# Optimization experiments

Hardware: AMD Instinct MI355X
Metric: run time of the kernel (lower is better)

The kernel has to match this reference:

```python
import jax, jax.numpy as jnp
import numpy as np

N = 50000        # nodes
E = 800000       # edges (before self-loops)
IN_DIM = 128
OUT_DIM = 128
HEADS = 4
HEAD_DIM = OUT_DIM // HEADS
NEG_SLOPE = 0.2  # GATv2Conv default negative_slope
LN_EPS = 1e-5


def setup_inputs() -> dict:
    key = jax.random.key(0)
    ks = jax.random.split(key, 6)
    def glorot(k, shape, fan):
        return jax.random.normal(k, shape, jnp.float32) * (1.0 / np.sqrt(fan))
    x = jax.random.normal(ks[0], (N, IN_DIM), jnp.float32)
    edge_index = jax.random.randint(ks[1], (2, E), 0, N, dtype=jnp.int32)
    W_l = glorot(ks[2], (IN_DIM, OUT_DIM), IN_DIM)   # lin_l (source/message transform)
    W_r = glorot(ks[3], (IN_DIM, OUT_DIM), IN_DIM)   # lin_r (target transform)
    att = glorot(ks[4], (HEADS, HEAD_DIM), HEAD_DIM)  # per-head attention vector a
    bias = jnp.zeros((OUT_DIM,), jnp.float32)
    gamma = jnp.ones((OUT_DIM,), jnp.float32)
    beta = jnp.zeros((OUT_DIM,), jnp.float32)
    return {"x": x, "edge_index": edge_index, "W_l": W_l, "W_r": W_r,
            "att": att, "bias": bias, "gamma": gamma, "beta": beta}


def reference(x, edge_index, W_l, W_r, att, bias, gamma, beta):
    # --- GATv2Conv (PyG defaults: add_self_loops=True, share_weights=False) ---
    loop = jnp.arange(N, dtype=edge_index.dtype)
    src = jnp.concatenate([edge_index[0], loop])  # message sources j
    dst = jnp.concatenate([edge_index[1], loop])  # message targets i

    xl = (x @ W_l).reshape(N, HEADS, HEAD_DIM)  # source-side features
    xr = (x @ W_r).reshape(N, HEADS, HEAD_DIM)  # target-side features

    h = xl[src] + xr[dst]                                  # [E+N, H, D]
    h = jnp.where(h > 0, h, NEG_SLOPE * h)                 # LeakyReLU
    logits = jnp.einsum('ehd,hd->eh', h, att)              # [E+N, H]

    # segment softmax over incoming edges of each target node
    m = jax.ops.segment_max(logits, dst, num_segments=N)   # [N, H]
    p = jnp.exp(logits - m[dst])
    s = jax.ops.segment_sum(p, dst, num_segments=N)        # [N, H]
    alpha = p / s[dst]                                     # [E+N, H]

    out = jax.ops.segment_sum(alpha[:, :, None] * xl[src], dst, num_segments=N)
    out = out.reshape(N, OUT_DIM) + bias                   # concat heads + bias

    # --- ELU + LayerNorm ---
    out = jax.nn.elu(out)
    mu = jnp.mean(out, axis=-1, keepdims=True)
    var = jnp.var(out, axis=-1, keepdims=True)
    out = (out - mu) / jnp.sqrt(var + LN_EPS) * gamma + beta
    return out
```

## Files before the change

### kernel.cpp

```cpp
#include <hip/hip_runtime.h>

#define IN_DIM   128
#define OUT_DIM  128
#define HEADS    4
#define HEAD_DIM 32
#define NEG_SLOPE 0.2f
#define LN_EPS    1e-5f
#define CAP      64
#define CAP_SH   6
#define BIN_EDGES 4096

typedef __bf16 bf16x8 __attribute__((ext_vector_type(8)));
typedef float  f32x4  __attribute__((ext_vector_type(4)));

__device__ __forceinline__ unsigned short f2bf(float f) {
    unsigned u = __float_as_uint(f);
    u += 0x7fffu + ((u >> 16) & 1u);
    return (unsigned short)(u >> 16);
}

__device__ __forceinline__ float2 bf2up(unsigned u) {
    return make_float2(__uint_as_float(u << 16), __uint_as_float(u & 0xffff0000u));
}
__device__ __forceinline__ float2 pk_add(float2 a, float2 b) {
    return make_float2(a.x + b.x, a.y + b.y);
}
__device__ __forceinline__ float2 pk_max(float2 a, float2 b) {
    return make_float2(fmaxf(a.x, b.x), fmaxf(a.y, b.y));
}
__device__ __forceinline__ float2 pk_muls(float2 a, float s) {
    return make_float2(a.x * s, a.y * s);
}
__device__ __forceinline__ float2 pk_fma(float2 a, float2 b, float2 c) {
    return make_float2(fmaf(a.x, b.x, c.x), fmaf(a.y, b.y, c.y));
}
__device__ __forceinline__ float2 pk_fmas(float s, float2 b, float2 c) {
    return make_float2(fmaf(s, b.x, c.x), fmaf(s, b.y, c.y));
}

__global__ void prep0(const float* __restrict__ Wl,
                      const float* __restrict__ Wr,
                      unsigned short* __restrict__ wpack,
                      int* __restrict__ cnt, int N) {
    const int tid = blockIdx.x * 256 + threadIdx.x;
    for (int i = tid; i < N + 8; i += 4096) cnt[i] = 0;

    const int lane = tid & 63;
    const int ks   = (tid >> 6) & 3;
    const int t    = tid >> 8;
    const int nt   = t & 7, half = t >> 3;
    const int n    = nt * 16 + (lane & 15);
    const int k0   = ks * 32 + (lane >> 4) * 8;
    const float* W = half ? Wr : Wl;
    union { unsigned short s[8]; uint4 q; } u;
    #pragma unroll
    for (int j = 0; j < 8; ++j) u.s[j] = f2bf(W[(k0 + j) * OUT_DIM + n]);
    ((uint4*)wpack)[tid] = u.q;
}

__global__ void bin_edges(const int* __restrict__ ei, int E, int N,
                          unsigned* __restrict__ buf, int bufstride,
                          int* __restrict__ pcur) {
    __shared__ int lhist[8], lbase[8];
    if (threadIdx.x < 8) lhist[threadIdx.x] = 0;
    __syncthreads();
    const int ET  = E + N;
    const int seg = blockIdx.x * BIN_EDGES;
    unsigned pr[16], rk[16];
    #pragma unroll
    for (int j = 0; j < 16; ++j) {
        const int e = seg + j * 256 + threadIdx.x;
        rk[j] = 0xffffffffu;
        if (e < ET) {
            int src, dst;
            if (e < E) { dst = ei[E + e]; src = ei[e]; }
            else       { dst = src = e - E; }
            const int p = dst >> 13;
            pr[j] = ((unsigned)dst << 16) | (unsigned)src;
            const int r = atomicAdd(&lhist[p], 1);
            rk[j] = ((unsigned)p << 16) | (unsigned)r;
        }
    }
    __syncthreads();
    if (threadIdx.x < 8)
        lbase[threadIdx.x] = atomicAdd(&pcur[threadIdx.x], lhist[threadIdx.x]);
    __syncthreads();
    #pragma unroll
    for (int j = 0; j < 16; ++j) {
        if (rk[j] != 0xffffffffu) {
            const int p = rk[j] >> 16, r = rk[j] & 0xffffu;
            buf[(size_t)p * bufstride + lbase[p] + r] = pr[j];
        }
    }
}

__global__ void scatter_gemm(const unsigned* __restrict__ buf, int bufstride,
                             const int* __restrict__ pcur,
                             int* __restrict__ cnt,
                             unsigned short* __restrict__ csr16,
                             const float* __restrict__ x,
                             const unsigned short* __restrict__ wpack,
                             unsigned short* __restrict__ xl,
                             unsigned short* __restrict__ xr,
                             int N) {
    if (blockIdx.x < 512) {
        const int p  = blockIdx.x & 7;
        const int bi = blockIdx.x >> 3;
        const int pc = pcur[p];
        const unsigned* b = buf + (size_t)p * bufstride;
        for (int i = bi * 256 + threadIdx.x; i < pc; i += 64 * 256) {
            const unsigned pair = b[i];
            const int dst = (int)(pair >> 16);
            const int src = (int)(pair & 0xffffu);
            const int pos = atomicAdd(&cnt[dst], 1);
            if (pos < CAP) csr16[(dst << CAP_SH) + pos] = (unsigned short)src;
        }
        return;
    }

    const int bid    = blockIdx.x - 512;
    const int wv     = threadIdx.x >> 6;
    const int lane   = threadIdx.x & 63;
    const int rowgrp = wv & 1, half = wv >> 1;
    const int r0     = bid * 32 + rowgrp * 16;
    const int m      = lane & 15, quad = lane >> 4;
    const int r      = r0 + m;
    unsigned short* out = half ? xr : xl;
    const uint4* wp = (const uint4*)wpack;

    f32x4 acc[8];
    #pragma unroll
    for (int nt = 0; nt < 8; ++nt) acc[nt] = (f32x4){0.f, 0.f, 0.f, 0.f};

    #pragma unroll
    for (int ks = 0; ks < 4; ++ks) {
        union { unsigned short s[8]; bf16x8 v; } af;
        if (r < N) {
            const float4* xp = (const float4*)(x + (size_t)r * IN_DIM + ks * 32 + quad * 8);
            float4 f0 = xp[0];
            float4 f1 = xp[1];
            af.s[0] = f2bf(f0.x); af.s[1] = f2bf(f0.y);
            af.s[2] = f2bf(f0.z); af.s[3] = f2bf(f0.w);
            af.s[4] = f2bf(f1.x); af.s[5] = f2bf(f1.y);
            af.s[6] = f2bf(f1.z); af.s[7] = f2bf(f1.w);
        } else {
            #pragma unroll
            for (int j = 0; j < 8; ++j) af.s[j] = 0;
        }
        #pragma unroll
        for (int nt = 0; nt < 8; ++nt) {
            union { uint4 q; bf16x8 v; } bf_;
            bf_.q = wp[((half * 8 + nt) * 4 + ks) * 64 + lane];
            acc[nt] = __builtin_amdgcn_mfma_f32_16x16x32_bf16(af.v, bf_.v, acc[nt], 0, 0, 0);
        }
    }

    #pragma unroll
    for (int nt = 0; nt < 8; ++nt) {
        #pragma unroll
        for (int i = 0; i < 4; ++i) {
            int gr = r0 + quad * 4 + i;
            if (gr < N) out[(size_t)gr * OUT_DIM + nt * 16 + m] = f2bf(acc[nt][i]);
        }
    }
}

__global__ void aggregate(const int* __restrict__ cnt,
                          const unsigned short* __restrict__ csr16,
                          const uint4* __restrict__ xlq,
                          const uint4* __restrict__ xrq,
                          const float* __restrict__ att,
                          const float* __restrict__ bias,
                          const float* __restrict__ gamma,
                          const float* __restrict__ beta,
                          float* __restrict__ out, int N) {
    const int node = (int)((blockIdx.x * (size_t)blockDim.x + threadIdx.x) >> 6);
    const int lane = threadIdx.x & 63;
    if (node >= N) return;
    const int slot = lane >> 4;
    const int sl   = lane & 15;

    int deg = cnt[node];
    deg = (deg > CAP) ? CAP : deg;
    const int beg = node << CAP_SH;

    const uint4 urq = xrq[(size_t)node * 16 + sl];
    float2 r2[4] = { bf2up(urq.x), bf2up(urq.y), bf2up(urq.z), bf2up(urq.w) };
    const float4 af0 = ((const float4*)att)[2 * sl];
    const float4 af1 = ((const float4*)att)[2 * sl + 1];
    float2 a2[4] = { make_float2(af0.x, af0.y), make_float2(af0.z, af0.w),
                     make_float2(af1.x, af1.y), make_float2(af1.z, af1.w) };

    float sden = 0.f;
    float2 acc2[4] = { make_float2(0.f, 0.f), make_float2(0.f, 0.f),
                       make_float2(0.f, 0.f), make_float2(0.f, 0.f) };

    const int sh = (slot & 1) << 4;
    for (int k = 0; k < deg; k += 8) {
        const uint4 cs = *(const uint4*)(csr16 + beg + k);
        const int id0 = (int)((((slot & 2) ? cs.y : cs.x) >> sh) & 0xffffu);
        const int id1 = (int)((((slot & 2) ? cs.w : cs.z) >> sh) & 0xffffu);
        const uint4 u0 = xlq[(size_t)id0 * 16 + sl];
        const uint4 u1 = xlq[(size_t)id1 * 16 + sl];
        float2 l0[4] = { bf2up(u0.x), bf2up(u0.y), bf2up(u0.z), bf2up(u0.w) };
        float2 l1[4] = { bf2up(u1.x), bf2up(u1.y), bf2up(u1.z), bf2up(u1.w) };
        float2 q0v = make_float2(0.f, 0.f), q1v = make_float2(0.f, 0.f);
        #pragma unroll
        for (int j = 0; j < 4; ++j) {
            float2 v0 = pk_add(l0[j], r2[j]);
            v0 = pk_max(v0, pk_muls(v0, NEG_SLOPE));
            q0v = pk_fma(v0, a2[j], q0v);
            float2 v1 = pk_add(l1[j], r2[j]);
            v1 = pk_max(v1, pk_muls(v1, NEG_SLOPE));
            q1v = pk_fma(v1, a2[j], q1v);
        }
        float q0 = q0v.x + q0v.y;
        float q1 = q1v.x + q1v.y;
        q0 += __shfl_xor(q0, 1, 64); q1 += __shfl_xor(q1, 1, 64);
        q0 += __shfl_xor(q0, 2, 64); q1 += __shfl_xor(q1, 2, 64);
        const float pe0 = (k + slot     < deg) ? __expf(q0) : 0.f;
        const float pe1 = (k + 4 + slot < deg) ? __expf(q1) : 0.f;
        sden += pe0 + pe1;
        #pragma unroll
        for (int j = 0; j < 4; ++j)
            acc2[j] = pk_fmas(pe1, l1[j], pk_fmas(pe0, l0[j], acc2[j]));
    }

    #pragma unroll
    for (int o = 16; o <= 32; o <<= 1) {
        sden += __shfl_xor(sden, o, 64);
        #pragma unroll
        for (int j = 0; j < 4; ++j) {
            acc2[j].x += __shfl_xor(acc2[j].x, o, 64);
            acc2[j].y += __shfl_xor(acc2[j].y, o, 64);
        }
    }

    const float inv_s = 1.f / sden;
    const float4 b0 = ((const float4*)bias)[2 * sl];
    const float4 b1 = ((const float4*)bias)[2 * sl + 1];
    const float bi[8] = {b0.x, b0.y, b0.z, b0.w, b1.x, b1.y, b1.z, b1.w};
    const float ac[8] = {acc2[0].x, acc2[0].y, acc2[1].x, acc2[1].y,
                         acc2[2].x, acc2[2].y, acc2[3].x, acc2[3].y};
    float v[8];
    float sum = 0.f, ssq = 0.f;
    #pragma unroll
    for (int j = 0; j < 8; ++j) {
        float t = ac[j] * inv_s + bi[j];
        t = (t > 0.f) ? t : (__expf(t) - 1.f);
        v[j] = t;
        sum += t;
        ssq = fmaf(t, t, ssq);
    }
    #pragma unroll
    for (int o = 1; o <= 8; o <<= 1) {
        sum += __shfl_xor(sum, o, 64);
        ssq += __shfl_xor(ssq, o, 64);
    }
    const float mean = sum * (1.f / 128.f);
    const float var  = ssq * (1.f / 128.f) - mean * mean;
    const float inv  = rsqrtf(var + LN_EPS);
    if (slot == 0) {
        const float4 g0 = ((const float4*)gamma)[2 * sl];
        const float4 g1 = ((const float4*)gamma)[2 * sl + 1];
        const float4 t0 = ((const float4*)beta)[2 * sl];
        const float4 t1 = ((const float4*)beta)[2 * sl + 1];
        float4 o0, o1;
        o0.x = (v[0] - mean) * inv * g0.x + t0.x;
        o0.y = (v[1] - mean) * inv * g0.y + t0.y;
        o0.z = (v[2] - mean) * inv * g0.z + t0.z;
        o0.w = (v[3] - mean) * inv * g0.w + t0.w;
        o1.x = (v[4] - mean) * inv * g1.x + t1.x;
        o1.y = (v[5] - mean) * inv * g1.y + t1.y;
        o1.z = (v[6] - mean) * inv * g1.z + t1.z;
        o1.w = (v[7] - mean) * inv * g1.w + t1.w;
        float4* orow = (float4*)(out + (size_t)node * OUT_DIM);
        orow[2 * sl]     = o0;
        orow[2 * sl + 1] = o1;
    }
}

extern "C" void kernel_launch(void* const* d_in, const int* in_sizes, int n_in,
                              void* d_out, int out_size, void* d_ws, size_t ws_size,
                              hipStream_t stream) {
    const float* x     = (const float*)d_in[0];
    const int*   ei    = (const int*)  d_in[1];
    const float* Wl    = (const float*)d_in[2];
    const float* Wr    = (const float*)d_in[3];
    const float* att   = (const float*)d_in[4];
    const float* bias  = (const float*)d_in[5];
    const float* gamma = (const float*)d_in[6];
    const float* beta  = (const float*)d_in[7];
    float* out = (float*)d_out;

    const int N  = in_sizes[0] / IN_DIM;
    const int E  = in_sizes[1] / 2;
    const int ET = E + N;

    char* ws = (char*)d_ws;
    unsigned short* xl    = (unsigned short*)ws;
    unsigned short* xr    = xl + (size_t)N * OUT_DIM;
    unsigned short* wpack = xr + (size_t)N * OUT_DIM;
    unsigned short* csr16 = wpack + 32768;
    int* cnt = (int*)(csr16 + (size_t)N * CAP);
    int* pcur = cnt + N;
    unsigned* buf = (unsigned*)(pcur + 8);

    prep0<<<16, 256, 0, stream>>>(Wl, Wr, wpack, cnt, N);

    const int binB = (ET + BIN_EDGES - 1) / BIN_EDGES;
    bin_edges<<<binB, 256, 0, stream>>>(ei, E, N, buf, ET, pcur);

    const int gemmB = (N + 31) / 32;
    scatter_gemm<<<512 + gemmB, 256, 0, stream>>>(buf, ET, pcur, cnt, csr16,
                                                  x, wpack, xl, xr, N);

    aggregate<<<(N + 3) / 4, 256, 0, stream>>>(
        cnt, csr16, (const uint4*)xl, (const uint4*)xr,
        att, bias, gamma, beta, out, N);
}
```

Before: 196.3 us.

## Prefetch neighbor features in aggregate, fold weight repack into binning kernel

The aggregate loop now loads all 64 neighbor ids for a node once per lane and distributes them by shuffle. It also software-pipelines the gather of the next 8 neighbors' source features so they are fetched while the current batch is computed. The separate prep kernel is removed: counters are zeroed with a memset, and the weight bf16 repack runs as extra blocks appended to the edge-binning launch. The intent is to hide gather latency and cut one launch, at the cost of more registers in aggregate that may lower occupancy.

```diff
diff --git a/kernel.cpp b/kernel.cpp
--- a/kernel.cpp
+++ b/kernel.cpp
@@ -38,29 +38,28 @@
     return make_float2(fmaf(s, b.x, c.x), fmaf(s, b.y, c.y));
 }
 
-__global__ void prep0(const float* __restrict__ Wl,
-                      const float* __restrict__ Wr,
-                      unsigned short* __restrict__ wpack,
-                      int* __restrict__ cnt, int N) {
-    const int tid = blockIdx.x * 256 + threadIdx.x;
-    for (int i = tid; i < N + 8; i += 4096) cnt[i] = 0;
-
-    const int lane = tid & 63;
-    const int ks   = (tid >> 6) & 3;
-    const int t    = tid >> 8;
-    const int nt   = t & 7, half = t >> 3;
-    const int n    = nt * 16 + (lane & 15);
-    const int k0   = ks * 32 + (lane >> 4) * 8;
-    const float* W = half ? Wr : Wl;
-    union { unsigned short s[8]; uint4 q; } u;
-    #pragma unroll
-    for (int j = 0; j < 8; ++j) u.s[j] = f2bf(W[(k0 + j) * OUT_DIM + n]);
-    ((uint4*)wpack)[tid] = u.q;
-}
-
-__global__ void bin_edges(const int* __restrict__ ei, int E, int N,
-                          unsigned* __restrict__ buf, int bufstride,
-                          int* __restrict__ pcur) {
+__global__ void bin_repack(const int* __restrict__ ei, int E, int N,
+                           unsigned* __restrict__ buf, int bufstride,
+                           int* __restrict__ pcur,
+                           const float* __restrict__ Wl,
+                           const float* __restrict__ Wr,
+                           unsigned short* __restrict__ wpack, int binB) {
+    if ((int)blockIdx.x >= binB) {
+        const int tid  = (blockIdx.x - binB) * 256 + threadIdx.x;
+        const int lane = tid & 63;
+        const int ks   = (tid >> 6) & 3;
+        const int t    = tid >> 8;
+        const int nt   = t & 7, half = t >> 3;
+        const int n    = nt * 16 + (lane & 15);
+        const int k0   = ks * 32 + (lane >> 4) * 8;
+        const float* W = half ? Wr : Wl;
+        union { unsigned short s[8]; uint4 q; } u;
+        #pragma unroll
+        for (int j = 0; j < 8; ++j) u.s[j] = f2bf(W[(k0 + j) * OUT_DIM + n]);
+        ((uint4*)wpack)[tid] = u.q;
+        return;
+    }
+
     __shared__ int lhist[8], lbase[8];
     if (threadIdx.x < 8) lhist[threadIdx.x] = 0;
     __syncthreads();
@@ -184,6 +183,8 @@
     deg = (deg > CAP) ? CAP : deg;
     const int beg = node << CAP_SH;
 
+    const int myid = (int)csr16[beg + lane];
+
     const uint4 urq = xrq[(size_t)node * 16 + sl];
     float2 r2[4] = { bf2up(urq.x), bf2up(urq.y), bf2up(urq.z), bf2up(urq.w) };
     const float4 af0 = ((const float4*)att)[2 * sl];
@@ -195,13 +196,20 @@
     float2 acc2[4] = { make_float2(0.f, 0.f), make_float2(0.f, 0.f),
                        make_float2(0.f, 0.f), make_float2(0.f, 0.f) };
 
-    const int sh = (slot & 1) << 4;
+    int id0 = __shfl(myid, slot, 64);
+    int id1 = __shfl(myid, 4 + slot, 64);
+    uint4 u0 = xlq[(size_t)id0 * 16 + sl];
+    uint4 u1 = xlq[(size_t)id1 * 16 + sl];
+
     for (int k = 0; k < deg; k += 8) {
-        const uint4 cs = *(const uint4*)(csr16 + beg + k);
-        const int id0 = (int)((((slot & 2) ? cs.y : cs.x) >> sh) & 0xffffu);
-        const int id1 = (int)((((slot & 2) ? cs.w : cs.z) >> sh) & 0xffffu);
-        const uint4 u0 = xlq[(size_t)id0 * 16 + sl];
-        const uint4 u1 = xlq[(size_t)id1 * 16 + sl];
+        uint4 u0n = u0, u1n = u1;
+        if (k + 8 < deg) {
+            const int id0n = __shfl(myid, k + 8 + slot, 64);
+            const int id1n = __shfl(myid, k + 12 + slot, 64);
+            u0n = xlq[(size_t)id0n * 16 + sl];
+            u1n = xlq[(size_t)id1n * 16 + sl];
+        }
+
         float2 l0[4] = { bf2up(u0.x), bf2up(u0.y), bf2up(u0.z), bf2up(u0.w) };
         float2 l1[4] = { bf2up(u1.x), bf2up(u1.y), bf2up(u1.z), bf2up(u1.w) };
         float2 q0v = make_float2(0.f, 0.f), q1v = make_float2(0.f, 0.f);
@@ -224,6 +232,8 @@
         #pragma unroll
         for (int j = 0; j < 4; ++j)
             acc2[j] = pk_fmas(pe1, l1[j], pk_fmas(pe0, l0[j], acc2[j]));
+
+        u0 = u0n; u1 = u1n;
     }
 
     #pragma unroll
@@ -306,10 +316,11 @@
     int* pcur = cnt + N;
     unsigned* buf = (unsigned*)(pcur + 8);
 
-    prep0<<<16, 256, 0, stream>>>(Wl, Wr, wpack, cnt, N);
+    hipMemsetAsync(cnt, 0, (size_t)(N + 8) * sizeof(int), stream);
 
     const int binB = (ET + BIN_EDGES - 1) / BIN_EDGES;
-    bin_edges<<<binB, 256, 0, stream>>>(ei, E, N, buf, ET, pcur);
+    bin_repack<<<binB + 16, 256, 0, stream>>>(ei, E, N, buf, ET, pcur,
+                                              Wl, Wr, wpack, binB);
 
     const int gemmB = (N + 31) / 32;
     scatter_gemm<<<512 + gemmB, 256, 0, stream>>>(buf, ET, pcur, cnt, csr16,
```

New measurement: 191.5 us. 1.03x faster.
